# Performance work log

Hardware: AMD Instinct MI355X
Metric: run time of the kernel (lower is better)

## Reference

```python
import jax, jax.numpy as jnp
import numpy as np

B, N1, N2 = 16, 4096, 1024
C1, C2 = 128, 256
IN_CH, OUT_CH = 4096, 256  # fc1 acts on N1 dim due to transpose; BN channels = C2 = OUT_CH
BN_EPS = 1e-5


def setup_inputs() -> dict:
    key = jax.random.key(0)
    ks = jax.random.split(key, 8)
    x1 = jax.random.normal(ks[0], (B, N1, C1), dtype=jnp.float32)
    x2 = jax.random.normal(ks[1], (B, N2, C2), dtype=jnp.float32)
    xyz1 = jax.random.normal(ks[2], (B, N1, 3), dtype=jnp.float32)
    xyz2 = jax.random.normal(ks[3], (B, N2, 3), dtype=jnp.float32)
    # Linear(in_channels=N1 -> out_channels) params, PyTorch default init scale
    bound = 1.0 / np.sqrt(IN_CH)
    W1 = jax.random.uniform(ks[4], (OUT_CH, IN_CH), jnp.float32, -bound, bound)
    b1 = jax.random.uniform(ks[5], (OUT_CH,), jnp.float32, -bound, bound)
    gamma = jnp.ones((OUT_CH,), jnp.float32)
    beta = jnp.zeros((OUT_CH,), jnp.float32)
    return {"x1": x1, "x2": x2, "xyz1": xyz1, "xyz2": xyz2,
            "W1": W1, "b1": b1, "gamma": gamma, "beta": beta}


def _square_distance(src, dst):
    # src: [B,N,3], dst: [B,M,3] -> [B,N,M]
    d = -2.0 * jnp.einsum('bnc,bmc->bnm', src, dst)
    d = d + jnp.sum(src * src, -1)[:, :, None]
    d = d + jnp.sum(dst * dst, -1)[:, None, :]
    return d


def reference(x1, x2, xyz1, xyz2, W1, b1, gamma, beta):
    dists = _square_distance(xyz1, xyz2)              # [B,N1,N2]
    neg3, idx = jax.lax.top_k(-dists, 3)              # 3 smallest distances
    d3 = -neg3                                        # [B,N1,3], ascending
    dist_recip = 1.0 / (d3 + 1e-8)
    weight = dist_recip / jnp.sum(dist_recip, axis=2, keepdims=True)
    gathered = jax.vmap(lambda pts, i: pts[i])(x2, idx)   # [B,N1,3,C2]
    interp = jnp.sum(gathered * weight[..., None], axis=2)  # [B,N1,C2]
    t = jnp.swapaxes(interp, 1, 2)                    # [B,C2,N1]
    y = jnp.einsum('bcn,on->bco', t, W1) + b1         # [B,C2,OUT_CH]
    # BatchNorm1d over channel dim 1 (size C2 == OUT_CH), training-mode batch stats
    mean = jnp.mean(y, axis=(0, 2), keepdims=True)
    var = jnp.mean((y - mean) ** 2, axis=(0, 2), keepdims=True)
    y = (y - mean) / jnp.sqrt(var + BN_EPS)
    y = gamma[None, :, None] * y + beta[None, :, None]
    y = jax.nn.relu(y)
    return jnp.swapaxes(y, 1, 2)                      # [B,OUT_CH,C2]
```

## Files before the change

### kernel.cpp

```cpp
#include <hip/hip_runtime.h>
#include <hip/hip_bf16.h>
#include <float.h>

#define B_    16
#define N1_   4096
#define N2_   1024
#define C2_   256
#define OUT_  256
#define K_    4096
#define SPLITK 8
#define KCH_  (K_ / SPLITK)
#define ZSLAB 1048576

typedef short short8 __attribute__((ext_vector_type(8)));
typedef float float4v __attribute__((ext_vector_type(4)));

static __device__ __forceinline__ unsigned short f32_to_bf16_bits(float v) {
    __hip_bfloat16 h = __float2bfloat16(v);
    return *(unsigned short*)&h;
}

__global__ __launch_bounds__(256) void w1cvt_kernel(
    const float* __restrict__ W1, unsigned short* __restrict__ W1b,
    float* __restrict__ accum)
{
    if (blockIdx.x == 0) {
        accum[threadIdx.x] = 0.0f;
        accum[256 + threadIdx.x] = 0.0f;
    }
    const int i = (blockIdx.x * 256 + threadIdx.x) * 4;
    float4 v = *(const float4*)(W1 + i);
    ushort4 o;
    o.x = f32_to_bf16_bits(v.x);
    o.y = f32_to_bf16_bits(v.y);
    o.z = f32_to_bf16_bits(v.z);
    o.w = f32_to_bf16_bits(v.w);
    *(ushort4*)(W1b + i) = o;
}

#define TPAD 65
struct KnnSh {
    float4 pts[N2_];
    float  pf[4][64][3];
};
union ShUnion {
    KnnSh a;
    unsigned short tile[C2_][TPAD];
};

__global__ __launch_bounds__(256) void knn_interp_kernel(
    const float* __restrict__ xyz1,
    const float* __restrict__ xyz2,
    const float* __restrict__ x2,
    unsigned short* __restrict__ interp_t)
{
    __shared__ ShUnion sh;
    __shared__ float rw[64][3];
    __shared__ int   ri[64][3];

    const int b  = blockIdx.y;
    const int n0 = blockIdx.x * 64;
    const int t  = threadIdx.x;
    const int w  = t >> 6;
    const int l  = t & 63;

    for (int r = 0; r < 4; ++r) {
        int j = r * 256 + t;
        const float* p = xyz2 + ((size_t)b * N2_ + j) * 3;
        float x = p[0], y = p[1], z = p[2];
        sh.a.pts[j] = make_float4(x, y, z, 0.5f * ((x * x + y * y) + z * z));
    }
    __syncthreads();

    const int n1 = n0 + l;
    const float* q = xyz1 + ((size_t)b * N1_ + n1) * 3;
    const float s0 = q[0], s1 = q[1], s2 = q[2];
    const float ns0 = -s0, ns1 = -s1, ns2 = -s2;
    const float ss = (s0 * s0 + s1 * s1) + s2 * s2;

    const int jbase = w << 8;
    float f0 = FLT_MAX, f1 = FLT_MAX, f2 = FLT_MAX;

    #pragma unroll 4
    for (int jj = 0; jj < 256; ++jj) {
        const int j = jbase + jj;
        float4 pq = sh.a.pts[j];
        float acc = fmaf(ns0, pq.x, pq.w);
        acc = fmaf(ns1, pq.y, acc);
        acc = fmaf(ns2, pq.z, acc);
        float dk = fmaxf(fmaf(2.0f, acc, ss), 0.0f);
        float fp = __int_as_float((__float_as_int(dk) & 0xFFFFFC00) | j);
        float nf0 = fminf(fp, f0);
        float nf1 = __builtin_amdgcn_fmed3f(fp, f0, f1);
        float nf2 = fminf(f2, fmaxf(fp, f1));
        f0 = nf0; f1 = nf1; f2 = nf2;
    }

    sh.a.pf[w][l][0] = f0; sh.a.pf[w][l][1] = f1; sh.a.pf[w][l][2] = f2;
    __syncthreads();

    if (w == 0) {
        float g0 = FLT_MAX, g1 = FLT_MAX, g2 = FLT_MAX;
        #pragma unroll
        for (int p = 0; p < 4; ++p)
        #pragma unroll
        for (int r = 0; r < 3; ++r) {
            float fp = sh.a.pf[p][l][r];
            float n0v = fminf(fp, g0);
            float n1v = __builtin_amdgcn_fmed3f(fp, g0, g1);
            float n2v = fminf(g2, fmaxf(fp, g1));
            g0 = n0v; g1 = n1v; g2 = n2v;
        }
        int j0 = __float_as_int(g0) & 1023;
        int j1 = __float_as_int(g1) & 1023;
        int j2 = __float_as_int(g2) & 1023;
        const float4 p0 = sh.a.pts[j0];
        const float4 p1 = sh.a.pts[j1];
        const float4 p2 = sh.a.pts[j2];
        float d0 = ss + 2.0f * (p0.w - ((s0 * p0.x + s1 * p0.y) + s2 * p0.z));
        float d1 = ss + 2.0f * (p1.w - ((s0 * p1.x + s1 * p1.y) + s2 * p1.z));
        float d2 = ss + 2.0f * (p2.w - ((s0 * p2.x + s1 * p2.y) + s2 * p2.z));
        float r0 = 1.0f / (d0 + 1e-8f);
        float r1 = 1.0f / (d1 + 1e-8f);
        float r2 = 1.0f / (d2 + 1e-8f);
        float s  = (r0 + r1) + r2;
        rw[l][0] = r0 / s;  rw[l][1] = r1 / s;  rw[l][2] = r2 / s;
        ri[l][0] = j0;      ri[l][1] = j1;      ri[l][2] = j2;
    }
    __syncthreads();

    for (int p = 0; p < 16; ++p) {
        int nl = p * 4 + w;
        float w0 = rw[nl][0], w1 = rw[nl][1], w2 = rw[nl][2];
        int i0g = ri[nl][0], i1g = ri[nl][1], i2g = ri[nl][2];
        const float4 va = ((const float4*)(x2 + ((size_t)b * N2_ + i0g) * C2_))[l];
        const float4 vb = ((const float4*)(x2 + ((size_t)b * N2_ + i1g) * C2_))[l];
        const float4 vc = ((const float4*)(x2 + ((size_t)b * N2_ + i2g) * C2_))[l];
        float fa[4] = {va.x, va.y, va.z, va.w};
        float fb[4] = {vb.x, vb.y, vb.z, vb.w};
        float fc[4] = {vc.x, vc.y, vc.z, vc.w};
        #pragma unroll
        for (int i = 0; i < 4; ++i) {
            float v = w0 * fa[i];
            v = fmaf(w1, fb[i], v);
            v = fmaf(w2, fc[i], v);
            sh.tile[l * 4 + i][nl] = f32_to_bf16_bits(v);
        }
    }
    __syncthreads();

    for (int r = 0; r < 64; ++r) {
        int c = r * 4 + w;
        interp_t[((size_t)b * C2_ + c) * K_ + n0 + l] = sh.tile[c][l];
    }
}

#define LDA 40
__global__ __launch_bounds__(256) void gemm_kernel(
    const unsigned short* __restrict__ W1b,
    const unsigned short* __restrict__ interp_t,
    float* __restrict__ Zp)
{
    __shared__ unsigned short Alds[128][LDA];
    __shared__ unsigned short Blds[64][LDA];
    const int z  = blockIdx.z;
    const int b  = z >> 3;
    const int kc = z & 7;
    const int o0 = blockIdx.y * 128;
    const int c0 = blockIdx.x * 64;
    const int t = threadIdx.x;
    const int w = t >> 6, l = t & 63;
    const int arow = t >> 1, ahalf = t & 1;
    const int brow = t >> 2, bq = t & 3;
    const int ob = (w >> 1) * 64, cb = (w & 1) * 32;
    const int m = l & 15, kq = l >> 4;

    const unsigned short* Wp = W1b + (size_t)(o0 + arow) * K_ + kc * KCH_ + ahalf * 16;
    const unsigned short* Bp = interp_t + ((size_t)b * C2_ + (c0 + brow)) * K_ + kc * KCH_ + bq * 8;

    float4v acc[4][2] = {};

    for (int kk = 0; kk < KCH_; kk += 32) {
        uint4 av0 = *(const uint4*)(Wp + kk);
        uint4 av1 = *(const uint4*)(Wp + kk + 8);
        uint4 bv  = *(const uint4*)(Bp + kk);
        *(uint4*)&Alds[arow][ahalf * 16]     = av0;
        *(uint4*)&Alds[arow][ahalf * 16 + 8] = av1;
        *(uint4*)&Blds[brow][bq * 8]         = bv;
        __syncthreads();
        short8 bf0 = *(const short8*)&Blds[cb + m][kq * 8];
        short8 bf1 = *(const short8*)&Blds[cb + 16 + m][kq * 8];
        #pragma unroll
        for (int mi = 0; mi < 4; ++mi) {
            short8 af = *(const short8*)&Alds[ob + mi * 16 + m][kq * 8];
            acc[mi][0] = __builtin_amdgcn_mfma_f32_16x16x32_bf16(af, bf0, acc[mi][0], 0, 0, 0);
            acc[mi][1] = __builtin_amdgcn_mfma_f32_16x16x32_bf16(af, bf1, acc[mi][1], 0, 0, 0);
        }
        __syncthreads();
    }

    float* Zslab = Zp + (size_t)kc * ZSLAB;
    #pragma unroll
    for (int mi = 0; mi < 4; ++mi)
    #pragma unroll
    for (int ni = 0; ni < 2; ++ni)
    #pragma unroll
    for (int r = 0; r < 4; ++r) {
        int o = o0 + ob + mi * 16 + kq * 4 + r;
        int c = c0 + cb + ni * 16 + m;
        Zslab[((size_t)b * OUT_ + o) * C2_ + c] = acc[mi][ni][r];
    }
}

__global__ __launch_bounds__(256) void reduce_stats_kernel(
    float* __restrict__ Zp, const float* __restrict__ b1,
    float* __restrict__ accum)
{
    const int b  = blockIdx.x >> 4;
    const int oq = blockIdx.x & 15;
    const int c  = threadIdx.x;
    float s = 0.0f, s2 = 0.0f;
    for (int o16 = 0; o16 < 16; ++o16) {
        int o = oq * 16 + o16;
        size_t base = ((size_t)b * OUT_ + o) * C2_ + c;
        float v = b1[o];
        #pragma unroll
        for (int sl = 0; sl < SPLITK; ++sl)
            v += Zp[base + (size_t)sl * ZSLAB];
        Zp[base] = v;
        s += v; s2 += v * v;
    }
    atomicAdd(&accum[c], s);
    atomicAdd(&accum[C2_ + c], s2);
}

__global__ __launch_bounds__(256) void bn_kernel(
    const float* __restrict__ Z, const float* __restrict__ accum,
    const float* __restrict__ gamma, const float* __restrict__ beta,
    float* __restrict__ out)
{
    const int i = (blockIdx.x * 256 + threadIdx.x) * 4;
    float4 z = *(const float4*)(Z + i);
    float vals[4] = {z.x, z.y, z.z, z.w};
    const int cb = i & 255;
    float res[4];
    #pragma unroll
    for (int j = 0; j < 4; ++j) {
        int c = cb + j;
        float mean = accum[c] * (1.0f / 4096.0f);
        float var  = accum[C2_ + c] * (1.0f / 4096.0f) - mean * mean;
        float rstd = 1.0f / sqrtf(var + 1e-5f);
        float v = gamma[c] * ((vals[j] - mean) * rstd) + beta[c];
        res[j] = fmaxf(v, 0.0f);
    }
    *(float4*)(out + i) = make_float4(res[0], res[1], res[2], res[3]);
}

extern "C" void kernel_launch(void* const* d_in, const int* in_sizes, int n_in,
                              void* d_out, int out_size, void* d_ws, size_t ws_size,
                              hipStream_t stream) {
    const float* x2    = (const float*)d_in[1];
    const float* xyz1  = (const float*)d_in[2];
    const float* xyz2  = (const float*)d_in[3];
    const float* W1    = (const float*)d_in[4];
    const float* b1    = (const float*)d_in[5];
    const float* gamma = (const float*)d_in[6];
    const float* beta  = (const float*)d_in[7];

    char* ws = (char*)d_ws;
    unsigned short* interp_t = (unsigned short*)(ws);
    unsigned short* W1b      = (unsigned short*)(ws + 33554432);
    float*          Zp       = (float*)(ws + 35651584);
    float*          accum    = (float*)(ws + 69206016);

    w1cvt_kernel      <<<1024, 256, 0, stream>>>(W1, W1b, accum);
    knn_interp_kernel <<<dim3(64, 16), 256, 0, stream>>>(xyz1, xyz2, x2, interp_t);
    gemm_kernel       <<<dim3(4, 2, 128), 256, 0, stream>>>(W1b, interp_t, Zp);
    reduce_stats_kernel<<<256, 256, 0, stream>>>(Zp, b1, accum);
    bn_kernel         <<<1024, 256, 0, stream>>>(Zp, accum, gamma, beta,
                                                 (float*)d_out);
}
```

Baseline: 163.0 us.

## Fuse W1 conversion into KNN kernel and prefetch GEMM tiles with K-step 64

Folds the W1 fp32-to-bf16 conversion and accumulator zeroing into the KNN/interpolation launch as 1024 extra blocks, removing one kernel launch and letting that work overlap the KNN blocks. The GEMM now stages 64-wide K tiles (LDS row pitch 72) and issues the global loads for the next tile into registers while MFMAs run on the current one. This halves the number of barrier pairs per K chunk at the cost of more registers and LDS. A KNN block that does not fit alongside the conversion blocks could change occupancy.

```diff
diff --git a/kernel.cpp b/kernel.cpp
--- a/kernel.cpp
+++ b/kernel.cpp
@@ -20,24 +20,6 @@
     return *(unsigned short*)&h;
 }
 
-__global__ __launch_bounds__(256) void w1cvt_kernel(
-    const float* __restrict__ W1, unsigned short* __restrict__ W1b,
-    float* __restrict__ accum)
-{
-    if (blockIdx.x == 0) {
-        accum[threadIdx.x] = 0.0f;
-        accum[256 + threadIdx.x] = 0.0f;
-    }
-    const int i = (blockIdx.x * 256 + threadIdx.x) * 4;
-    float4 v = *(const float4*)(W1 + i);
-    ushort4 o;
-    o.x = f32_to_bf16_bits(v.x);
-    o.y = f32_to_bf16_bits(v.y);
-    o.z = f32_to_bf16_bits(v.z);
-    o.w = f32_to_bf16_bits(v.w);
-    *(ushort4*)(W1b + i) = o;
-}
-
 #define TPAD 65
 struct KnnSh {
     float4 pts[N2_];
@@ -52,17 +34,39 @@
     const float* __restrict__ xyz1,
     const float* __restrict__ xyz2,
     const float* __restrict__ x2,
-    unsigned short* __restrict__ interp_t)
+    unsigned short* __restrict__ interp_t,
+    const float* __restrict__ W1,
+    unsigned short* __restrict__ W1b,
+    float* __restrict__ accum)
 {
     __shared__ ShUnion sh;
     __shared__ float rw[64][3];
     __shared__ int   ri[64][3];
 
-    const int b  = blockIdx.y;
-    const int n0 = blockIdx.x * 64;
-    const int t  = threadIdx.x;
-    const int w  = t >> 6;
-    const int l  = t & 63;
+    const int bid = blockIdx.x;
+    const int t   = threadIdx.x;
+
+    if (bid < 1024) {
+        if (bid == 0) {
+            accum[t] = 0.0f;
+            accum[256 + t] = 0.0f;
+        }
+        const int i = (bid * 256 + t) * 4;
+        float4 v = *(const float4*)(W1 + i);
+        ushort4 o;
+        o.x = f32_to_bf16_bits(v.x);
+        o.y = f32_to_bf16_bits(v.y);
+        o.z = f32_to_bf16_bits(v.z);
+        o.w = f32_to_bf16_bits(v.w);
+        *(ushort4*)(W1b + i) = o;
+        return;
+    }
+
+    const int rem = bid - 1024;
+    const int b   = rem >> 6;
+    const int n0  = (rem & 63) * 64;
+    const int w   = t >> 6;
+    const int l   = t & 63;
 
     for (int r = 0; r < 4; ++r) {
         int j = r * 256 + t;
@@ -155,7 +159,7 @@
     }
 }
 
-#define LDA 40
+#define LDA 72
 __global__ __launch_bounds__(256) void gemm_kernel(
     const unsigned short* __restrict__ W1b,
     const unsigned short* __restrict__ interp_t,
@@ -175,26 +179,46 @@
     const int ob = (w >> 1) * 64, cb = (w & 1) * 32;
     const int m = l & 15, kq = l >> 4;
 
-    const unsigned short* Wp = W1b + (size_t)(o0 + arow) * K_ + kc * KCH_ + ahalf * 16;
-    const unsigned short* Bp = interp_t + ((size_t)b * C2_ + (c0 + brow)) * K_ + kc * KCH_ + bq * 8;
+    const unsigned short* Wp = W1b + (size_t)(o0 + arow) * K_ + kc * KCH_ + ahalf * 32;
+    const unsigned short* Bp = interp_t + ((size_t)b * C2_ + (c0 + brow)) * K_ + kc * KCH_ + bq * 16;
 
     float4v acc[4][2] = {};
 
-    for (int kk = 0; kk < KCH_; kk += 32) {
-        uint4 av0 = *(const uint4*)(Wp + kk);
-        uint4 av1 = *(const uint4*)(Wp + kk + 8);
-        uint4 bv  = *(const uint4*)(Bp + kk);
-        *(uint4*)&Alds[arow][ahalf * 16]     = av0;
-        *(uint4*)&Alds[arow][ahalf * 16 + 8] = av1;
-        *(uint4*)&Blds[brow][bq * 8]         = bv;
+    uint4 a0 = *(const uint4*)(Wp);
+    uint4 a1 = *(const uint4*)(Wp + 8);
+    uint4 a2 = *(const uint4*)(Wp + 16);
+    uint4 a3 = *(const uint4*)(Wp + 24);
+    uint4 b0 = *(const uint4*)(Bp);
+    uint4 b1 = *(const uint4*)(Bp + 8);
+
+    for (int kk = 0; kk < KCH_; kk += 64) {
+        *(uint4*)&Alds[arow][ahalf * 32]      = a0;
+        *(uint4*)&Alds[arow][ahalf * 32 + 8]  = a1;
+        *(uint4*)&Alds[arow][ahalf * 32 + 16] = a2;
+        *(uint4*)&Alds[arow][ahalf * 32 + 24] = a3;
+        *(uint4*)&Blds[brow][bq * 16]         = b0;
+        *(uint4*)&Blds[brow][bq * 16 + 8]     = b1;
         __syncthreads();
-        short8 bf0 = *(const short8*)&Blds[cb + m][kq * 8];
-        short8 bf1 = *(const short8*)&Blds[cb + 16 + m][kq * 8];
-        #pragma unroll
-        for (int mi = 0; mi < 4; ++mi) {
-            short8 af = *(const short8*)&Alds[ob + mi * 16 + m][kq * 8];
-            acc[mi][0] = __builtin_amdgcn_mfma_f32_16x16x32_bf16(af, bf0, acc[mi][0], 0, 0, 0);
-            acc[mi][1] = __builtin_amdgcn_mfma_f32_16x16x32_bf16(af, bf1, acc[mi][1], 0, 0, 0);
+
+        if (kk + 64 < KCH_) {
+            a0 = *(const uint4*)(Wp + kk + 64);
+            a1 = *(const uint4*)(Wp + kk + 72);
+            a2 = *(const uint4*)(Wp + kk + 80);
+            a3 = *(const uint4*)(Wp + kk + 88);
+            b0 = *(const uint4*)(Bp + kk + 64);
+            b1 = *(const uint4*)(Bp + kk + 72);
+        }
+
+        #pragma unroll
+        for (int ks = 0; ks < 64; ks += 32) {
+            short8 bf0 = *(const short8*)&Blds[cb + m][ks + kq * 8];
+            short8 bf1 = *(const short8*)&Blds[cb + 16 + m][ks + kq * 8];
+            #pragma unroll
+            for (int mi = 0; mi < 4; ++mi) {
+                short8 af = *(const short8*)&Alds[ob + mi * 16 + m][ks + kq * 8];
+                acc[mi][0] = __builtin_amdgcn_mfma_f32_16x16x32_bf16(af, bf0, acc[mi][0], 0, 0, 0);
+                acc[mi][1] = __builtin_amdgcn_mfma_f32_16x16x32_bf16(af, bf1, acc[mi][1], 0, 0, 0);
+            }
         }
         __syncthreads();
     }
@@ -273,8 +297,8 @@
     float*          Zp       = (float*)(ws + 35651584);
     float*          accum    = (float*)(ws + 69206016);
 
-    w1cvt_kernel      <<<1024, 256, 0, stream>>>(W1, W1b, accum);
-    knn_interp_kernel <<<dim3(64, 16), 256, 0, stream>>>(xyz1, xyz2, x2, interp_t);
+    knn_interp_kernel <<<2048, 256, 0, stream>>>(xyz1, xyz2, x2, interp_t,
+                                                 W1, W1b, accum);
     gemm_kernel       <<<dim3(4, 2, 128), 256, 0, stream>>>(W1b, interp_t, Zp);
     reduce_stats_kernel<<<256, 256, 0, stream>>>(Zp, b1, accum);
     bn_kernel         <<<1024, 256, 0, stream>>>(Zp, accum, gamma, beta,
```

New measurement: 159.2 us. 1.02x faster.
